# Kernel tuning notes

Hardware: AMD Instinct MI355X
Metric: run time of the kernel (lower is better)

The kernel has to match this reference:

```python
import jax, jax.numpy as jnp
import numpy as np

D = 1024
H = 16
DFF = 4096
EPS = 1e-5


def layernorm(x, g, b):
    m = jnp.mean(x, axis=-1, keepdims=True)
    v = jnp.var(x, axis=-1, keepdims=True)
    return (x - m) * jax.lax.rsqrt(v + EPS) * g + b


def setup_inputs() -> dict:
    key = jax.random.key(0)
    ks = jax.random.split(key, 6)
    B, T = 2, 2048
    s = 0.02
    return {
        "x": jax.random.normal(ks[0], (B, T, D), dtype=jnp.float32),
        "W_qkv": jax.random.normal(ks[1], (D, 3 * D), dtype=jnp.float32) * s,
        "W_proj": jax.random.normal(ks[2], (D, D), dtype=jnp.float32) * s,
        "W_fc1": jax.random.normal(ks[3], (D, DFF), dtype=jnp.float32) * s,
        "W_fc2": jax.random.normal(ks[4], (DFF, D), dtype=jnp.float32) * s,
        "ln1_g": jnp.ones((D,), jnp.float32),
        "ln1_b": jnp.zeros((D,), jnp.float32),
        "ln2_g": jnp.ones((D,), jnp.float32),
        "ln2_b": jnp.zeros((D,), jnp.float32),
    }


def reference(x, W_qkv, W_proj, W_fc1, W_fc2, ln1_g, ln1_b, ln2_g, ln2_b):
    B, T, C = x.shape
    hd = C // H

    # --- attention sublayer (pre-norm) ---
    h = layernorm(x, ln1_g, ln1_b)
    qkv = h @ W_qkv                                  # [B,T,3C]
    q, k, v = jnp.split(qkv, 3, axis=-1)
    q = q.reshape(B, T, H, hd).transpose(0, 2, 1, 3)  # [B,H,T,hd]
    k = k.reshape(B, T, H, hd).transpose(0, 2, 1, 3)
    v = v.reshape(B, T, H, hd).transpose(0, 2, 1, 3)
    att = jnp.einsum('bhqd,bhkd->bhqk', q, k) * (1.0 / np.sqrt(hd))
    causal = jnp.tril(jnp.ones((T, T), dtype=bool))
    att = jnp.where(causal, att, jnp.float32(-jnp.inf))
    att = jax.nn.softmax(att, axis=-1)
    y = jnp.einsum('bhqk,bhkd->bhqd', att, v)        # [B,H,T,hd]
    y = y.transpose(0, 2, 1, 3).reshape(B, T, C)
    x = x + y @ W_proj

    # --- MLP sublayer (pre-norm) ---
    h = layernorm(x, ln2_g, ln2_b)
    h = jax.nn.gelu(h @ W_fc1, approximate=False)
    x = x + h @ W_fc2
    return x
```

## Files before the change

kernel.cpp:

```cpp
#include <hip/hip_runtime.h>
#include <hip/hip_bf16.h>
#include <math.h>

typedef __bf16 bf16;
typedef __bf16 bf16x4 __attribute__((ext_vector_type(4)));
typedef __bf16 bf16x8 __attribute__((ext_vector_type(8)));
typedef float f32x4 __attribute__((ext_vector_type(4)));
typedef unsigned int u32;

#define MFMA_BF16(a, b, c) __builtin_amdgcn_mfma_f32_16x16x32_bf16(a, b, c, 0, 0, 0)
#define ASYNC16(g, l)                                                                   \
    __builtin_amdgcn_global_load_lds((const __attribute__((address_space(1))) u32*)(g), \
                                     (__attribute__((address_space(3))) u32*)(l), 16, 0, 0)

__global__ __launch_bounds__(256)
void transpose_cast(const float* __restrict__ in, bf16* __restrict__ out, int rows, int cols) {
    __shared__ float tile[32][33];
    const int tx = threadIdx.x, ty = threadIdx.y;
    const int c0 = blockIdx.x * 32, r0 = blockIdx.y * 32;
    #pragma unroll
    for (int j = 0; j < 4; j++)
        tile[ty + j * 8][tx] = in[(size_t)(r0 + ty + j * 8) * cols + c0 + tx];
    __syncthreads();
    #pragma unroll
    for (int j = 0; j < 4; j++)
        out[(size_t)(c0 + ty + j * 8) * rows + r0 + tx] = (bf16)tile[tx][ty + j * 8];
}

__global__ __launch_bounds__(256)
void transpose_v(const bf16* __restrict__ qkv, bf16* __restrict__ vt) {
    __shared__ bf16 tile[32][33];
    const int tx = threadIdx.x, ty = threadIdx.y;
    const int t0 = blockIdx.x * 32;
    const int d0 = blockIdx.y * 32;
    const int bh = blockIdx.z;
    const int b = bh >> 4, h = bh & 15;
    const bf16* src = qkv + (size_t)b * 2048 * 3072 + 2048 + h * 64;
    #pragma unroll
    for (int j = 0; j < 4; j++)
        tile[ty + j * 8][tx] = src[(size_t)(t0 + ty + j * 8) * 3072 + d0 + tx];
    __syncthreads();
    #pragma unroll
    for (int j = 0; j < 4; j++)
        vt[((size_t)bh * 64 + d0 + ty + j * 8) * 2048 + t0 + tx] = tile[tx][ty + j * 8];
}

__global__ __launch_bounds__(256)
void ln_kernel(const float* __restrict__ x, const float* __restrict__ g,
               const float* __restrict__ bb, bf16* __restrict__ out) {
    const int row = blockIdx.x, tid = threadIdx.x;
    const float4 v = reinterpret_cast<const float4*>(x)[(size_t)row * 256 + tid];
    float s = v.x + v.y + v.z + v.w;
    float sq = v.x * v.x + v.y * v.y + v.z * v.z + v.w * v.w;
    #pragma unroll
    for (int o = 32; o > 0; o >>= 1) { s += __shfl_xor(s, o); sq += __shfl_xor(sq, o); }
    __shared__ float ssum[4], ssq[4];
    const int wave = tid >> 6, lane = tid & 63;
    if (lane == 0) { ssum[wave] = s; ssq[wave] = sq; }
    __syncthreads();
    s = ssum[0] + ssum[1] + ssum[2] + ssum[3];
    sq = ssq[0] + ssq[1] + ssq[2] + ssq[3];
    const float mean = s * (1.0f / 1024.0f);
    const float var = sq * (1.0f / 1024.0f) - mean * mean;
    const float rstd = rsqrtf(var + 1e-5f);
    const float4 gv = reinterpret_cast<const float4*>(g)[tid];
    const float4 bv = reinterpret_cast<const float4*>(bb)[tid];
    bf16x4 o;
    o[0] = (bf16)((v.x - mean) * rstd * gv.x + bv.x);
    o[1] = (bf16)((v.y - mean) * rstd * gv.y + bv.y);
    o[2] = (bf16)((v.z - mean) * rstd * gv.z + bv.z);
    o[3] = (bf16)((v.w - mean) * rstd * gv.w + bv.w);
    reinterpret_cast<bf16x4*>(out)[(size_t)row * 256 + tid] = o;
}

__device__ __forceinline__ float gelu_fast(float v) {
    const float vv = v * v;
    const float u = v * (1.595769122f + 0.0713548162726f * vv);
    const float t = exp2f(u * -1.4426950408889634f);
    return v / (1.0f + t);
}

template <int EPI>
__global__ __launch_bounds__(256)
void gemm_bt(const bf16* __restrict__ A, const bf16* __restrict__ Bt,
             bf16* __restrict__ outb, int M, int N, int K) {
    __shared__ bf16 As[3][128][32];
    __shared__ bf16 Bs[3][128][32];
    const int tid = threadIdx.x;
    const int wave = tid >> 6, lane = tid & 63;
    const int lm = lane & 15, lq = lane >> 4;
    const int wm = (wave >> 1) * 64, wn = (wave & 1) * 64;
    const int bm = blockIdx.y * 128, bn = blockIdx.x * 128;
    const int srow = lane >> 2;
    const int sg = (((lane & 3) ^ ((lane >> 3) & 3)) * 8);
    const int pco = (lq ^ ((lm >> 1) & 3)) * 8;
    f32x4 acc[4][4];
    #pragma unroll
    for (int i = 0; i < 4; i++)
        #pragma unroll
        for (int j = 0; j < 4; j++) acc[i][j] = (f32x4){0.f, 0.f, 0.f, 0.f};

    auto stage = [&](int bb, int kt) {
        ASYNC16(A + (size_t)(bm + wave * 32 + srow) * K + kt + sg,      &As[bb][wave * 32][0]);
        ASYNC16(A + (size_t)(bm + wave * 32 + 16 + srow) * K + kt + sg, &As[bb][wave * 32 + 16][0]);
        ASYNC16(Bt + (size_t)(bn + wave * 32 + srow) * K + kt + sg,      &Bs[bb][wave * 32][0]);
        ASYNC16(Bt + (size_t)(bn + wave * 32 + 16 + srow) * K + kt + sg, &Bs[bb][wave * 32 + 16][0]);
    };

    const int NT = K >> 5;
    stage(0, 0);
    stage(1, 32);
    asm volatile("s_waitcnt vmcnt(4)" ::: "memory");
    __builtin_amdgcn_s_barrier();
    __builtin_amdgcn_sched_barrier(0);

    int cur = 0;
    for (int t = 0; t < NT; ++t) {
        if (t + 2 < NT) {
            const int nxt2 = (cur == 0) ? 2 : cur - 1;
            stage(nxt2, (t + 2) * 32);
        }
        bf16x8 af[4], bfr[4];
        #pragma unroll
        for (int i = 0; i < 4; i++)
            af[i] = *reinterpret_cast<const bf16x8*>(&As[cur][wm + i * 16 + lm][pco]);
        #pragma unroll
        for (int j = 0; j < 4; j++)
            bfr[j] = *reinterpret_cast<const bf16x8*>(&Bs[cur][wn + j * 16 + lm][pco]);
        #pragma unroll
        for (int i = 0; i < 4; i++)
            #pragma unroll
            for (int j = 0; j < 4; j++)
                acc[i][j] = MFMA_BF16(af[i], bfr[j], acc[i][j]);

        if (t + 1 < NT) {
            if (t + 2 < NT) asm volatile("s_waitcnt vmcnt(4)" ::: "memory");
            else            asm volatile("s_waitcnt vmcnt(0)" ::: "memory");
            __builtin_amdgcn_s_barrier();
            __builtin_amdgcn_sched_barrier(0);
        }
        cur = (cur == 2) ? 0 : cur + 1;
    }

    const int r0 = bm + wm, c0 = bn + wn;
    #pragma unroll
    for (int i = 0; i < 4; i++)
        #pragma unroll
        for (int j = 0; j < 4; j++)
            #pragma unroll
            for (int e = 0; e < 4; e++) {
                const int row = r0 + i * 16 + lq * 4 + e;
                const int col = c0 + j * 16 + lm;
                const float v = acc[i][j][e];
                const size_t idx = (size_t)row * N + col;
                if (EPI == 0) outb[idx] = (bf16)v;
                else          outb[idx] = (bf16)gelu_fast(v);
            }
}

__global__ __launch_bounds__(256)
void gemm_bt64(const bf16* __restrict__ A, const bf16* __restrict__ Bt,
               const float* __restrict__ resid, float* __restrict__ outf,
               int M, int N, int K) {
    __shared__ bf16 As[2][128][64];
    __shared__ bf16 Bs[2][64][64];
    const int tid = threadIdx.x;
    const int wave = tid >> 6, lane = tid & 63;
    const int lm = lane & 15, lq = lane >> 4;
    const int wm = (wave >> 1) * 64, wn = (wave & 1) * 32;
    const int bm = blockIdx.y * 128, bn = blockIdx.x * 64;
    const int lr8 = lane >> 3;
    const int lg  = ((lane & 7) ^ lr8) * 8;
    const int sa  = lm & 7;
    int co[2];
    co[0] = (lq ^ sa) * 8;
    co[1] = ((lq ^ 4) ^ sa) * 8;
    f32x4 acc[4][2];
    #pragma unroll
    for (int i = 0; i < 4; i++)
        #pragma unroll
        for (int j = 0; j < 2; j++) acc[i][j] = (f32x4){0.f, 0.f, 0.f, 0.f};

    auto stage = [&](int bb, int kt) {
        #pragma unroll
        for (int s = 0; s < 4; s++)
            ASYNC16(A + (size_t)(bm + wave * 32 + s * 8 + lr8) * K + kt + lg, &As[bb][wave * 32 + s * 8][0]);
        #pragma unroll
        for (int s = 0; s < 2; s++)
            ASYNC16(Bt + (size_t)(bn + wave * 16 + s * 8 + lr8) * K + kt + lg, &Bs[bb][wave * 16 + s * 8][0]);
    };

    stage(0, 0);
    int cur = 0;
    for (int kt = 0; kt < K; kt += 64) {
        __syncthreads();
        if (kt + 64 < K) stage(cur ^ 1, kt + 64);
        bf16x8 af[2][4], bfr[2][2];
        #pragma unroll
        for (int kk = 0; kk < 2; kk++) {
            #pragma unroll
            for (int i = 0; i < 4; i++)
                af[kk][i] = *reinterpret_cast<const bf16x8*>(&As[cur][wm + i * 16 + lm][co[kk]]);
            #pragma unroll
            for (int j = 0; j < 2; j++)
                bfr[kk][j] = *reinterpret_cast<const bf16x8*>(&Bs[cur][wn + j * 16 + lm][co[kk]]);
        }
        #pragma unroll
        for (int kk = 0; kk < 2; kk++)
            #pragma unroll
            for (int i = 0; i < 4; i++)
                #pragma unroll
                for (int j = 0; j < 2; j++)
                    acc[i][j] = MFMA_BF16(af[kk][i], bfr[kk][j], acc[i][j]);
        cur ^= 1;
    }

    const int r0 = bm + wm, c0 = bn + wn;
    #pragma unroll
    for (int i = 0; i < 4; i++)
        #pragma unroll
        for (int j = 0; j < 2; j++)
            #pragma unroll
            for (int e = 0; e < 4; e++) {
                const int row = r0 + i * 16 + lq * 4 + e;
                const int col = c0 + j * 16 + lm;
                const size_t idx = (size_t)row * N + col;
                outf[idx] = resid[idx] + acc[i][j][e];
            }
}

__global__ __launch_bounds__(256)
void attn_kernel(const bf16* __restrict__ qkv, const bf16* __restrict__ vt,
                 bf16* __restrict__ y) {
    __shared__ bf16 Ks[64][68];
    __shared__ bf16 Vt[64][68];
    __shared__ bf16 Ps[4][16][68];
    const int tid = threadIdx.x, wave = tid >> 6, lane = tid & 63;
    const int lm = lane & 15, lq = lane >> 4;
    const int h = blockIdx.y, b = blockIdx.z;
    const size_t base = (size_t)b * 2048 * 3072;
    const bf16* Kbase = qkv + base + 1024 + h * 64;
    const bf16* Vbase = vt + ((size_t)(b * 16 + h) * 64) * 2048;
    const int skey = tid >> 3, sch = (tid & 7) * 8;
    const float k1 = 0.18033688011112042f;

    bf16x8 ones;
    #pragma unroll
    for (int j = 0; j < 8; j++) ones[j] = (lm == 0) ? (bf16)1.0f : (bf16)0.0f;

    for (int ph = 0; ph < 2; ph++) {
        const int qt = ph ? (int)blockIdx.x : 31 - (int)blockIdx.x;

        const int qrow = qt * 64 + wave * 16 + lm;
        const bf16* qp = qkv + base + (size_t)qrow * 3072 + h * 64 + lq * 8;
        bf16x8 aq0 = *reinterpret_cast<const bf16x8*>(qp);
        bf16x8 aq1 = *reinterpret_cast<const bf16x8*>(qp + 32);
        #pragma unroll
        for (int j = 0; j < 8; j++) {
            aq0[j] = (bf16)((float)aq0[j] * k1);
            aq1[j] = (bf16)((float)aq1[j] * k1);
        }

        f32x4 Oc[4], Ol;
        #pragma unroll
        for (int nt = 0; nt < 4; nt++) Oc[nt] = (f32x4){0.f, 0.f, 0.f, 0.f};
        Ol = (f32x4){0.f, 0.f, 0.f, 0.f};

        bf16x8 pk0, pk1, pv0, pv1;
        {
            const bf16* kp = Kbase + (size_t)skey * 3072 + sch;
            pk0 = *reinterpret_cast<const bf16x8*>(kp);
            pk1 = *reinterpret_cast<const bf16x8*>(kp + (size_t)32 * 3072);
            const bf16* vp = Vbase + (size_t)skey * 2048 + sch;
            pv0 = *reinterpret_cast<const bf16x8*>(vp);
            pv1 = *reinterpret_cast<const bf16x8*>(vp + (size_t)32 * 2048);
        }

        for (int kt2 = 0; kt2 <= qt; kt2++) {
            __syncthreads();
            *reinterpret_cast<bf16x8*>(&Ks[skey][sch])      = pk0;
            *reinterpret_cast<bf16x8*>(&Ks[skey + 32][sch]) = pk1;
            *reinterpret_cast<bf16x8*>(&Vt[skey][sch])      = pv0;
            *reinterpret_cast<bf16x8*>(&Vt[skey + 32][sch]) = pv1;
            __syncthreads();
            if (kt2 < qt) {
                const bf16* kp = Kbase + (size_t)((kt2 + 1) * 64 + skey) * 3072 + sch;
                pk0 = *reinterpret_cast<const bf16x8*>(kp);
                pk1 = *reinterpret_cast<const bf16x8*>(kp + (size_t)32 * 3072);
                const bf16* vp = Vbase + (size_t)skey * 2048 + (kt2 + 1) * 64 + sch;
                pv0 = *reinterpret_cast<const bf16x8*>(vp);
                pv1 = *reinterpret_cast<const bf16x8*>(vp + (size_t)32 * 2048);
            }

            f32x4 Sc[4];
            #pragma unroll
            for (int nt = 0; nt < 4; nt++) Sc[nt] = (f32x4){0.f, 0.f, 0.f, 0.f};
            #pragma unroll
            for (int nt = 0; nt < 4; nt++) {
                const bf16x8 bk0 = *reinterpret_cast<const bf16x8*>(&Ks[nt * 16 + lm][lq * 8]);
                const bf16x8 bk1 = *reinterpret_cast<const bf16x8*>(&Ks[nt * 16 + lm][32 + lq * 8]);
                Sc[nt] = MFMA_BF16(aq0, bk0, Sc[nt]);
                Sc[nt] = MFMA_BF16(aq1, bk1, Sc[nt]);
            }

            const int qb = wave * 16 + lq * 4;
            #pragma unroll
            for (int e = 0; e < 4; e++) {
                #pragma unroll
                for (int nt = 0; nt < 4; nt++) {
                    float sv = Sc[nt][e];
                    if (kt2 == qt && (nt * 16 + lm) > (qb + e)) sv = -1e30f;
                    Ps[wave][lq * 4 + e][nt * 16 + lm] = (bf16)exp2f(sv);
                }
            }

            const bf16x8 ap0 = *reinterpret_cast<const bf16x8*>(&Ps[wave][lm][lq * 8]);
            const bf16x8 ap1 = *reinterpret_cast<const bf16x8*>(&Ps[wave][lm][32 + lq * 8]);
            Ol = MFMA_BF16(ap0, ones, Ol);
            Ol = MFMA_BF16(ap1, ones, Ol);
            #pragma unroll
            for (int nt = 0; nt < 4; nt++) {
                const bf16x8 bv0 = *reinterpret_cast<const bf16x8*>(&Vt[nt * 16 + lm][lq * 8]);
                const bf16x8 bv1 = *reinterpret_cast<const bf16x8*>(&Vt[nt * 16 + lm][32 + lq * 8]);
                Oc[nt] = MFMA_BF16(ap0, bv0, Oc[nt]);
                Oc[nt] = MFMA_BF16(ap1, bv1, Oc[nt]);
            }
        }

        const int qrow0 = qt * 64 + wave * 16 + lq * 4;
        float inv[4];
        #pragma unroll
        for (int e = 0; e < 4; e++) inv[e] = 1.0f / __shfl(Ol[e], lane & 48);
        #pragma unroll
        for (int nt = 0; nt < 4; nt++)
            #pragma unroll
            for (int e = 0; e < 4; e++) {
                const int row = qrow0 + e;
                y[((size_t)b * 2048 + row) * 1024 + h * 64 + nt * 16 + lm] = (bf16)(Oc[nt][e] * inv[e]);
            }
    }
}

extern "C" void kernel_launch(void* const* d_in, const int* in_sizes, int n_in,
                              void* d_out, int out_size, void* d_ws, size_t ws_size,
                              hipStream_t stream) {
    const float* x     = (const float*)d_in[0];
    const float* Wqkv  = (const float*)d_in[1];
    const float* Wproj = (const float*)d_in[2];
    const float* Wfc1  = (const float*)d_in[3];
    const float* Wfc2  = (const float*)d_in[4];
    const float* ln1g  = (const float*)d_in[5];
    const float* ln1b  = (const float*)d_in[6];
    const float* ln2g  = (const float*)d_in[7];
    const float* ln2b  = (const float*)d_in[8];
    float* out = (float*)d_out;
    char* ws = (char*)d_ws;

    bf16*  Wqkvt  = (bf16*)(ws);
    bf16*  Wprojt = (bf16*)(ws + 6291456);
    bf16*  Wfc1t  = (bf16*)(ws + 8388608);
    bf16*  Wfc2t  = (bf16*)(ws + 16777216);
    bf16*  hb     = (bf16*)(ws + 25165824);
    bf16*  vt     = (bf16*)(ws + 25165824);
    bf16*  qkv    = (bf16*)(ws + 33554432);
    bf16*  yb     = (bf16*)(ws + 58720256);
    float* x1     = (float*)(ws + 67108864);
    bf16*  h3     = (bf16*)(ws + 33554432);

    const dim3 tb(32, 8);
    transpose_cast<<<dim3(96, 32), tb, 0, stream>>>(Wqkv, Wqkvt, 1024, 3072);
    transpose_cast<<<dim3(32, 32), tb, 0, stream>>>(Wproj, Wprojt, 1024, 1024);
    transpose_cast<<<dim3(128, 32), tb, 0, stream>>>(Wfc1, Wfc1t, 1024, 4096);
    transpose_cast<<<dim3(32, 128), tb, 0, stream>>>(Wfc2, Wfc2t, 4096, 1024);

    ln_kernel<<<dim3(4096), dim3(256), 0, stream>>>(x, ln1g, ln1b, hb);
    gemm_bt<0><<<dim3(24, 32), dim3(256), 0, stream>>>(hb, Wqkvt, qkv, 4096, 3072, 1024);
    transpose_v<<<dim3(64, 2, 32), tb, 0, stream>>>(qkv, vt);
    attn_kernel<<<dim3(16, 16, 2), dim3(256), 0, stream>>>(qkv, vt, yb);
    gemm_bt64<<<dim3(16, 32), dim3(256), 0, stream>>>(yb, Wprojt, x, x1, 4096, 1024, 1024);
    ln_kernel<<<dim3(4096), dim3(256), 0, stream>>>(x1, ln2g, ln2b, hb);
    gemm_bt<2><<<dim3(32, 32), dim3(256), 0, stream>>>(hb, Wfc1t, h3, 4096, 4096, 1024);
    gemm_bt64<<<dim3(16, 32), dim3(256), 0, stream>>>(h3, Wfc2t, x1, out, 4096, 1024, 4096);
}
```

Measured before the change: 352.0 us.

## Replace 128x128 GEMM with 256x256 tile, 8-wave ping-pong schedule

The QKV and FC1 GEMMs move from a 128x128, 4-wave, triple-buffered kernel to a 256x256, 8-wave kernel with a K-step of 64, double buffering, and four MFMA quadrants per iteration. Those quadrants are interleaved with LDS fragment loads and async global staging, separated by barriers and s_setprio. The goal is more operand reuse per LDS byte and better overlap of loads with MFMA work. The cost is far fewer blocks (192 and 256 on 256 CUs), which means wave quantization and idle CUs. It also adds high register pressure from the 32 accumulators under launch_bounds(512,2).

```diff
diff --git a/kernel.cpp b/kernel.cpp
--- a/kernel.cpp
+++ b/kernel.cpp
@@ -81,77 +81,134 @@
 }
 
 template <int EPI>
-__global__ __launch_bounds__(256)
-void gemm_bt(const bf16* __restrict__ A, const bf16* __restrict__ Bt,
+__global__ __launch_bounds__(512, 2)
+void gemm256(const bf16* __restrict__ A, const bf16* __restrict__ Bt,
              bf16* __restrict__ outb, int M, int N, int K) {
-    __shared__ bf16 As[3][128][32];
-    __shared__ bf16 Bs[3][128][32];
+    __shared__ bf16 As[2][2][2][128][32];
+    __shared__ bf16 Bs[2][2][2][128][32];
     const int tid = threadIdx.x;
     const int wave = tid >> 6, lane = tid & 63;
     const int lm = lane & 15, lq = lane >> 4;
-    const int wm = (wave >> 1) * 64, wn = (wave & 1) * 64;
-    const int bm = blockIdx.y * 128, bn = blockIdx.x * 128;
+    const int wr = wave >> 2, wc = wave & 3;
+    const int bm = blockIdx.y * 256, bn = blockIdx.x * 256;
     const int srow = lane >> 2;
     const int sg = (((lane & 3) ^ ((lane >> 3) & 3)) * 8);
     const int pco = (lq ^ ((lm >> 1) & 3)) * 8;
-    f32x4 acc[4][4];
-    #pragma unroll
-    for (int i = 0; i < 4; i++)
+
+    f32x4 acc[8][4];
+    #pragma unroll
+    for (int i = 0; i < 8; i++)
         #pragma unroll
         for (int j = 0; j < 4; j++) acc[i][j] = (f32x4){0.f, 0.f, 0.f, 0.f};
 
-    auto stage = [&](int bb, int kt) {
-        ASYNC16(A + (size_t)(bm + wave * 32 + srow) * K + kt + sg,      &As[bb][wave * 32][0]);
-        ASYNC16(A + (size_t)(bm + wave * 32 + 16 + srow) * K + kt + sg, &As[bb][wave * 32 + 16][0]);
-        ASYNC16(Bt + (size_t)(bn + wave * 32 + srow) * K + kt + sg,      &Bs[bb][wave * 32][0]);
-        ASYNC16(Bt + (size_t)(bn + wave * 32 + 16 + srow) * K + kt + sg, &Bs[bb][wave * 32 + 16][0]);
-    };
-
-    const int NT = K >> 5;
-    stage(0, 0);
-    stage(1, 32);
-    asm volatile("s_waitcnt vmcnt(4)" ::: "memory");
+    auto stageA = [&](int db, int kt) {
+        #pragma unroll
+        for (int L = 0; L < 2; L++) {
+            const int g = wave * 2 + L, slab = g >> 3, rg = g & 7;
+            #pragma unroll
+            for (int h = 0; h < 2; h++)
+                ASYNC16(A + (size_t)(bm + h * 128 + rg * 16 + srow) * K + kt + slab * 32 + sg,
+                        &As[db][h][slab][rg * 16][0]);
+        }
+    };
+    auto stageB = [&](int db, int kt) {
+        #pragma unroll
+        for (int L = 0; L < 2; L++) {
+            const int g = wave * 2 + L, slab = g >> 3, rg = g & 7;
+            #pragma unroll
+            for (int h = 0; h < 2; h++)
+                ASYNC16(Bt + (size_t)(bn + h * 128 + rg * 16 + srow) * K + kt + slab * 32 + sg,
+                        &Bs[db][h][slab][rg * 16][0]);
+        }
+    };
+    auto loadA = [&](int db, int mq, bf16x8 (&dst)[4][2]) {
+        #pragma unroll
+        for (int i = 0; i < 4; i++)
+            #pragma unroll
+            for (int kk = 0; kk < 2; kk++)
+                dst[i][kk] = *reinterpret_cast<const bf16x8*>(
+                    &As[db][wr][kk][(mq * 4 + i) * 16 + lm][pco]);
+    };
+    auto loadB = [&](int db, int bq, bf16x8 (&dst)[2][2]) {
+        #pragma unroll
+        for (int j = 0; j < 2; j++)
+            #pragma unroll
+            for (int kk = 0; kk < 2; kk++)
+                dst[j][kk] = *reinterpret_cast<const bf16x8*>(
+                    &Bs[db][wc >> 1][kk][(wc & 1) * 64 + (bq * 2 + j) * 16 + lm][pco]);
+    };
+    auto quad = [&](int mq, int bq, bf16x8 (&a)[4][2], bf16x8 (&b)[2][2]) {
+        #pragma unroll
+        for (int kk = 0; kk < 2; kk++)
+            #pragma unroll
+            for (int i = 0; i < 4; i++)
+                #pragma unroll
+                for (int j = 0; j < 2; j++)
+                    acc[mq * 4 + i][bq * 2 + j] =
+                        MFMA_BF16(a[i][kk], b[j][kk], acc[mq * 4 + i][bq * 2 + j]);
+    };
+
+#define PHASE_SYNC()                                         \
+    __builtin_amdgcn_s_barrier();                            \
+    asm volatile("s_waitcnt lgkmcnt(0)" ::: "memory");       \
+    __builtin_amdgcn_sched_barrier(0)
+
+    const int NT = K >> 6;
+    stageB(0, 0);  stageA(0, 0);
+    stageB(1, 64); stageA(1, 64);
+    asm volatile("s_waitcnt vmcnt(8)" ::: "memory");
     __builtin_amdgcn_s_barrier();
     __builtin_amdgcn_sched_barrier(0);
 
-    int cur = 0;
+    bf16x8 af[4][2], b0[2][2], b1[2][2];
     for (int t = 0; t < NT; ++t) {
+        const int db = t & 1;
+        const int kt2 = (t + 2) * 64;
+        loadA(db, 0, af);
+        loadB(db, 0, b0);
+        PHASE_SYNC();
+        __builtin_amdgcn_s_setprio(1);
+        quad(0, 0, af, b0);
+        __builtin_amdgcn_s_setprio(0);
+        __builtin_amdgcn_s_barrier();
+        loadB(db, 1, b1);
+        PHASE_SYNC();
+        __builtin_amdgcn_s_setprio(1);
+        quad(0, 1, af, b1);
+        __builtin_amdgcn_s_setprio(0);
+        __builtin_amdgcn_s_barrier();
+        loadA(db, 1, af);
+        if (t + 2 < NT) stageB(db, kt2);
+        PHASE_SYNC();
+        __builtin_amdgcn_s_setprio(1);
+        quad(1, 0, af, b0);
+        __builtin_amdgcn_s_setprio(0);
+        __builtin_amdgcn_s_barrier();
         if (t + 2 < NT) {
-            const int nxt2 = (cur == 0) ? 2 : cur - 1;
-            stage(nxt2, (t + 2) * 32);
-        }
-        bf16x8 af[4], bfr[4];
-        #pragma unroll
-        for (int i = 0; i < 4; i++)
-            af[i] = *reinterpret_cast<const bf16x8*>(&As[cur][wm + i * 16 + lm][pco]);
-        #pragma unroll
-        for (int j = 0; j < 4; j++)
-            bfr[j] = *reinterpret_cast<const bf16x8*>(&Bs[cur][wn + j * 16 + lm][pco]);
-        #pragma unroll
-        for (int i = 0; i < 4; i++)
-            #pragma unroll
-            for (int j = 0; j < 4; j++)
-                acc[i][j] = MFMA_BF16(af[i], bfr[j], acc[i][j]);
-
-        if (t + 1 < NT) {
-            if (t + 2 < NT) asm volatile("s_waitcnt vmcnt(4)" ::: "memory");
-            else            asm volatile("s_waitcnt vmcnt(0)" ::: "memory");
-            __builtin_amdgcn_s_barrier();
-            __builtin_amdgcn_sched_barrier(0);
-        }
-        cur = (cur == 2) ? 0 : cur + 1;
+            stageA(db, kt2);
+            asm volatile("s_waitcnt vmcnt(8)" ::: "memory");
+        } else if (t + 1 < NT) {
+            asm volatile("s_waitcnt vmcnt(0)" ::: "memory");
+        }
+        __builtin_amdgcn_s_barrier();
+        __builtin_amdgcn_sched_barrier(0);
+        __builtin_amdgcn_s_setprio(1);
+        quad(1, 1, af, b1);
+        __builtin_amdgcn_s_setprio(0);
+        __builtin_amdgcn_s_barrier();
     }
-
-    const int r0 = bm + wm, c0 = bn + wn;
-    #pragma unroll
-    for (int i = 0; i < 4; i++)
-        #pragma unroll
-        for (int j = 0; j < 4; j++)
+#undef PHASE_SYNC
+
+    const int r0 = bm + wr * 128, c0 = bn + wc * 64;
+    #pragma unroll
+    for (int mi = 0; mi < 8; mi++)
+        #pragma unroll
+        for (int ni = 0; ni < 4; ni++)
             #pragma unroll
             for (int e = 0; e < 4; e++) {
-                const int row = r0 + i * 16 + lq * 4 + e;
-                const int col = c0 + j * 16 + lm;
-                const float v = acc[i][j][e];
+                const int row = r0 + mi * 16 + lq * 4 + e;
+                const int col = c0 + ni * 16 + lm;
+                const float v = acc[mi][ni][e];
                 const size_t idx = (size_t)row * N + col;
                 if (EPI == 0) outb[idx] = (bf16)v;
                 else          outb[idx] = (bf16)gelu_fast(v);
@@ -374,11 +431,11 @@
     transpose_cast<<<dim3(32, 128), tb, 0, stream>>>(Wfc2, Wfc2t, 4096, 1024);
 
     ln_kernel<<<dim3(4096), dim3(256), 0, stream>>>(x, ln1g, ln1b, hb);
-    gemm_bt<0><<<dim3(24, 32), dim3(256), 0, stream>>>(hb, Wqkvt, qkv, 4096, 3072, 1024);
+    gemm256<0><<<dim3(12, 16), dim3(512), 0, stream>>>(hb, Wqkvt, qkv, 4096, 3072, 1024);
     transpose_v<<<dim3(64, 2, 32), tb, 0, stream>>>(qkv, vt);
     attn_kernel<<<dim3(16, 16, 2), dim3(256), 0, stream>>>(qkv, vt, yb);
     gemm_bt64<<<dim3(16, 32), dim3(256), 0, stream>>>(yb, Wprojt, x, x1, 4096, 1024, 1024);
     ln_kernel<<<dim3(4096), dim3(256), 0, stream>>>(x1, ln2g, ln2b, hb);
-    gemm_bt<2><<<dim3(32, 32), dim3(256), 0, stream>>>(hb, Wfc1t, h3, 4096, 4096, 1024);
+    gemm256<2><<<dim3(16, 16), dim3(512), 0, stream>>>(hb, Wfc1t, h3, 4096, 4096, 1024);
     gemm_bt64<<<dim3(16, 32), dim3(256), 0, stream>>>(h3, Wfc2t, x1, out, 4096, 1024, 4096);
 }
```

Result: faster. 343.3 us (-2.5%).
